# Optimization experiments

Hardware: AMD Instinct MI355X
Metric: run time of the kernel (lower is better)

The kernel has to match this reference:

```python
import jax, jax.numpy as jnp
import numpy as np

K = 32  # k-th nearest neighbor (excluding self), matches KDistanceDetector(k=32)


def setup_inputs() -> dict:
    key = jax.random.key(0)
    B, D = 16384, 128
    images = jax.random.normal(key, (B, D), dtype=jnp.float32)
    return {"images": images}


def reference(images):
    # model is identity: vision_features = images, shape [B, D]
    x = images
    # torch.cdist p=2 with mm path: sq dists via gram matrix
    sq_norms = jnp.sum(x * x, axis=1)                      # [B]
    sq = sq_norms[:, None] + sq_norms[None, :] - 2.0 * (x @ x.T)  # [B, B]
    sq = jnp.maximum(sq, 0.0)
    B = x.shape[0]
    # Mask out the diagonal (self-distance). Original removes it and views
    # [B, B-1]; setting it to +inf before sorting yields the identical k-th
    # smallest value (inf sorts last), and keeps sqrt grads clean.
    diag = jnp.eye(B, dtype=bool)
    sq = jnp.where(diag, jnp.inf, sq)
    d = jnp.sqrt(sq)                                       # [B, B]
    a = jnp.sort(d, axis=1)                                # full per-row sort, as in original
    return a[:, K]                                         # [B]
```

## Files before the change

### kernel.cpp

```cpp
#include <hip/hip_runtime.h>


typedef unsigned short u16;
typedef unsigned int   u32;
typedef __attribute__((ext_vector_type(8))) u16    ushort8;
typedef __attribute__((ext_vector_type(8))) __bf16 bf16x8;
typedef __attribute__((ext_vector_type(4))) float  f32x4;
typedef __attribute__((ext_vector_type(4))) u32    u32x4;

#define NB   16384
#define ND   128
#define NSEG 32
#define SCAP 12
#define NTH  33
#define ZWH  (-2.62f)
#define NEGF (-3.0e38f)
#define POSF ( 3.0e38f)
#define NPB  64
#define NPBL 256

#define OFF_X    ((size_t)0)
#define OFF_NORM (OFF_X    + (size_t)NB * ND * 2)
#define OFF_TACC (OFF_NORM + (size_t)NB * 4)
#define OFF_PART (OFF_TACC + (size_t)NB * 4)
#define OFF_CNTS (OFF_PART + (size_t)NPBL * 130 * 4)
#define OFF_CAND (OFF_CNTS + (size_t)NB * NSEG * 4)

static __device__ __forceinline__ u16 f2bf(float f) {
  u32 u = __float_as_uint(f);
  u32 r = u + 0x7FFFu + ((u >> 16) & 1u);
  return (u16)(r >> 16);
}
static __device__ __forceinline__ float bf2f(u16 h) {
  return __uint_as_float(((u32)h) << 16);
}

#if defined(__has_builtin)
#if __has_builtin(__builtin_amdgcn_global_load_lds)
#define HAVE_GLDS 1
#endif
#endif

static __device__ __forceinline__ void stage16(const u16* gsrc_lane,
                                               u16* lds_base, int l) {
#ifdef HAVE_GLDS
  __builtin_amdgcn_global_load_lds(
      (const __attribute__((address_space(1))) void*)gsrc_lane,
      (__attribute__((address_space(3))) void*)lds_base, 16, 0, 0);
#else
  *(ushort8*)(lds_base + l * 8) = *(const ushort8*)gsrc_lane;
#endif
}
static __device__ __forceinline__ void stage4(const float* gsrc_lane,
                                              float* lds_base, int l) {
#ifdef HAVE_GLDS
  __builtin_amdgcn_global_load_lds(
      (const __attribute__((address_space(1))) void*)gsrc_lane,
      (__attribute__((address_space(3))) void*)lds_base, 4, 0, 0);
#else
  lds_base[l] = *gsrc_lane;
#endif
}

__global__ void k_prepstats(const float* __restrict__ x, u16* __restrict__ X,
                            float* __restrict__ norms, float* __restrict__ partial) {
  __shared__ float xs[16][128];
  __shared__ float red1[256], red2[256];
  int t = threadIdx.x;
  int cg = t & 15;
  int rs = t >> 4;
  int rbase = blockIdx.x * NPB;
  float cs[8] = {0.f, 0.f, 0.f, 0.f, 0.f, 0.f, 0.f, 0.f};
  float s1 = 0.f, s2 = 0.f;
#pragma unroll
  for (int rr = 0; rr < NPB / 16; ++rr) {
    int row = rbase + rs + rr * 16;
    const float* src = x + (size_t)row * ND + cg * 8;
    float4 a0 = *(const float4*)(src);
    float4 a1 = *(const float4*)(src + 4);
    float v[8] = {a0.x, a0.y, a0.z, a0.w, a1.x, a1.y, a1.z, a1.w};
    ushort8 pack;
    float ns = 0.f;
#pragma unroll
    for (int u = 0; u < 8; ++u) {
      u16 h = f2bf(v[u]);
      float b = bf2f(h);
      pack[u] = h;
      ns += b * b;
      cs[u] += b;
    }
    *(ushort8*)(X + (size_t)row * ND + cg * 8) = pack;
#pragma unroll
    for (int off = 1; off < 16; off <<= 1) ns += __shfl_xor(ns, off, 64);
    if (cg == 0) { norms[row] = ns; s1 += ns; s2 += ns * ns; }
  }
#pragma unroll
  for (int u = 0; u < 8; ++u) xs[rs][cg * 8 + u] = cs[u];
  red1[t] = s1; red2[t] = s2;
  __syncthreads();
  if (t < 128) {
    float a = 0.f;
    for (int r2 = 0; r2 < 16; ++r2) a += xs[r2][t];
    partial[(size_t)blockIdx.x * 130 + t] = a;
  }
  for (int st = 128; st > 0; st >>= 1) {
    if (t < st) { red1[t] += red1[t + st]; red2[t] += red2[t + st]; }
    __syncthreads();
  }
  if (t == 0) {
    partial[(size_t)blockIdx.x * 130 + 128] = red1[0];
    partial[(size_t)blockIdx.x * 130 + 129] = red2[0];
  }
}

__global__ void k_thresh(const u16* __restrict__ X, const float* __restrict__ norms,
                         const float* __restrict__ partial, float* __restrict__ tacc) {
  __shared__ float xb[128];
  __shared__ float ssum[2];
  int t = threadIdx.x;
  if (t < 128) {
    float a = 0.f;
    for (int b = 0; b < NPBL; ++b) a += partial[(size_t)b * 130 + t];
    xb[t] = a * (1.0f / NB);
  } else if (t == 128 || t == 129) {
    float a = 0.f;
    for (int b = 0; b < NPBL; ++b) a += partial[(size_t)b * 130 + t];
    ssum[t - 128] = a;
  }
  __syncthreads();
  int r = blockIdx.x * 256 + t;
  float n = norms[r];
  const u16* xr = X + (size_t)r * ND;
  float dot = 0.f;
#pragma unroll
  for (int c8 = 0; c8 < 16; ++c8) {
    ushort8 v = *(const ushort8*)(xr + c8 * 8);
#pragma unroll
    for (int j = 0; j < 8; ++j) dot += bf2f(v[j]) * xb[c8 * 8 + j];
  }
  float nbar = ssum[0] * (1.0f / NB);
  float Vn = fmaxf(ssum[1] * (1.0f / NB) - nbar * nbar, 0.f);
  float m = n + nbar - 2.f * dot;
  float v = Vn + 4.f * n * (nbar / ND);
  float nu = 2.f * m * m / v;
  float cc = v / (2.f * m);
  float a1 = 2.f / (9.f * nu);
  float inner = 1.f - a1 + ZWH * sqrtf(a1);
  float tsq = cc * nu * inner * inner * inner;
  tacc[r] = 0.5f * (n - tsq);
}

__global__ __launch_bounds__(512, 4) void k_gram(
    const u16* __restrict__ X, const float* __restrict__ norms,
    const float* __restrict__ tacc, u32* __restrict__ counts,
    float* __restrict__ cands) {
  __shared__ u16 ldsA[2][32 * 512];
  __shared__ __align__(16) float nchs[2][128];
  const int bid = blockIdx.x;
  const int logical = (bid & 7) * 64 + (bid >> 3);
  const int q = logical >> 7, strip = logical & 127;
  const int r0 = strip * 128;
  const int t = threadIdx.x, w = t >> 6, l = t & 63;
  const int wr = w >> 1, wc = w & 1;
  const int lm = l & 15, lq = l >> 4;
  const int koff = lq * 8;

  bf16x8 bfrag[4][2];
#pragma unroll
  for (int k = 0; k < 4; ++k)
#pragma unroll
    for (int j = 0; j < 2; ++j)
      bfrag[k][j] = __builtin_bit_cast(bf16x8, *(const ushort8*)(
          X + (size_t)(r0 + wr * 32 + j * 16 + lm) * ND + k * 32 + koff));

  int rj[2]; float tj[2]; u32 cnt2[2]; u32 segb[2];
#pragma unroll
  for (int j = 0; j < 2; ++j) {
    rj[j] = r0 + wr * 32 + j * 16 + lm;
    tj[j] = tacc[rj[j]];
    cnt2[j] = 0;
    segb[j] = (u32)(rj[j] * NSEG + q * 8 + wc * 4 + lq) * SCAP;
  }

  {
    const int c0 = q * 4096;
#pragma unroll
    for (int s = 0; s < 4; ++s) {
      int g = w * 4 + s;
      stage16(X + (size_t)(c0 + (g & 7) * 16 + lm) * ND + (g >> 3) * 32 + koff,
              &ldsA[0][g * 512], l);
    }
    if (w < 2) stage4(norms + c0 + w * 64 + l, &nchs[0][w * 64], l);
  }
  __syncthreads();

  for (int it = 0; it < 32; ++it) {
    const int cur = it & 1;
    const int c0 = q * 4096 + it * 128;
    if (it + 1 < 32) {
      const int c1 = c0 + 128;
      u16* dstA = ldsA[cur ^ 1];
#pragma unroll
      for (int s = 0; s < 4; ++s) {
        int g = w * 4 + s;
        stage16(X + (size_t)(c1 + (g & 7) * 16 + lm) * ND + (g >> 3) * 32 + koff,
                &dstA[g * 512], l);
      }
      if (w < 2) stage4(norms + c1 + w * 64 + l, &nchs[cur ^ 1][w * 64], l);
    }
    __builtin_amdgcn_sched_barrier(0);

    f32x4 acc[4][2];
#pragma unroll
    for (int i = 0; i < 4; ++i)
#pragma unroll
      for (int j = 0; j < 2; ++j) acc[i][j] = (f32x4){0.f, 0.f, 0.f, 0.f};

    const u16* srcA = ldsA[cur];
#pragma unroll
    for (int k = 0; k < 4; ++k) {
      bf16x8 af[4];
#pragma unroll
      for (int i = 0; i < 4; ++i)
        af[i] = __builtin_bit_cast(bf16x8,
                 *(const ushort8*)(&srcA[(k * 8 + wc * 4 + i) * 512 + l * 8]));
#pragma unroll
      for (int i = 0; i < 4; ++i)
#pragma unroll
        for (int j = 0; j < 2; ++j)
          acc[i][j] = __builtin_amdgcn_mfma_f32_16x16x32_bf16(af[i], bfrag[k][j], acc[i][j], 0, 0, 0);
    }

    f32x4 nch4[4];
#pragma unroll
    for (int i = 0; i < 4; ++i) {
      nch4[i] = *(const f32x4*)(&nchs[cur][wc * 64 + i * 16 + lq * 4]);
      nch4[i] = nch4[i] * 0.5f;
    }

    const bool dg = (c0 == r0);
#pragma unroll
    for (int i = 0; i < 4; ++i) {
#pragma unroll
      for (int j = 0; j < 2; ++j) {
#pragma unroll
        for (int v = 0; v < 4; ++v) {
          float val = acc[i][j][v] - nch4[i][v];
          bool p = (val >= tj[j]);
          if (dg) p = p && ((c0 + wc * 64 + i * 16 + lq * 4 + v) != rj[j]);
          if (p) {
            u32 c = cnt2[j];
            if (c < SCAP) cands[segb[j] + c] = val;
            cnt2[j] = c + 1;
          }
        }
      }
    }

    __syncthreads();
  }
#pragma unroll
  for (int j = 0; j < 2; ++j)
    counts[rj[j] * NSEG + q * 8 + wc * 4 + lq] = cnt2[j];
}

__global__ void k_select(const u32* __restrict__ counts, const float* __restrict__ cands,
                         const float* __restrict__ norms, float* __restrict__ out) {
  int w = threadIdx.x >> 6, l = threadIdx.x & 63;
  int r = blockIdx.x * 4 + w;
  u32 myc = (l < NSEG) ? counts[r * NSEG + l] : 0u;
  u32 tot = myc, mx = myc;
#pragma unroll
  for (int off = 1; off < 64; off <<= 1) {
    tot += __shfl_xor(tot, off, 64);
    u32 o = (u32)__shfl_xor((int)mx, off, 64);
    mx = mx > o ? mx : o;
  }
  if (tot < NTH || mx > SCAP) return;

  const float* base = cands + (size_t)r * (NSEG * SCAP);
  float v0, v1, v2, v3, v4, v5;
#define LOADV(e, dst)                                        \
  {                                                          \
    int f = l + 64 * e;                                      \
    int sg = f / SCAP, sl = f - sg * SCAP;                   \
    u32 c = (u32)__shfl((int)myc, sg, 64);                   \
    float x = base[f];                                       \
    dst = (sl < (int)c) ? x : NEGF;                          \
  }
  LOADV(0, v0) LOADV(1, v1) LOADV(2, v2) LOADV(3, v3) LOADV(4, v4) LOADV(5, v5)
#undef LOADV

  float last = NEGF;
  for (int e = 0; e < NTH; ++e) {
    float m = fmaxf(fmaxf(fmaxf(v0, v1), fmaxf(v2, v3)), fmaxf(v4, v5));
#pragma unroll
    for (int off = 1; off < 64; off <<= 1) m = fmaxf(m, __shfl_xor(m, off, 64));
    bool mine = (v0 == m) || (v1 == m) || (v2 == m) || (v3 == m) || (v4 == m) || (v5 == m);
    unsigned long long bal = __ballot(mine);
    int owner = __ffsll(bal) - 1;
    if (l == owner) {
      if      (v0 == m) v0 = NEGF;
      else if (v1 == m) v1 = NEGF;
      else if (v2 == m) v2 = NEGF;
      else if (v3 == m) v3 = NEGF;
      else if (v4 == m) v4 = NEGF;
      else              v5 = NEGF;
    }
    last = m;
  }
  out[r] = sqrtf(fmaxf(norms[r] - 2.f * last, 0.f));
}

__global__ void k_fallback(const u32* __restrict__ counts, const u16* __restrict__ X,
                           const float* __restrict__ norms, float* __restrict__ out) {
  __shared__ float sq[NB];
  __shared__ float xr[ND];
  __shared__ float rmin[256];
  __shared__ int   ridx[256];
  __shared__ float tmin[256];
  __shared__ int   tidx[256];
  __shared__ int   nbad;
  __shared__ int   badlist[256];
  int t = threadIdx.x;
  if (t == 0) nbad = 0;
  __syncthreads();
  int r = blockIdx.x * 256 + t;
  u32 tot = 0, mx = 0;
#pragma unroll
  for (int s4 = 0; s4 < 8; ++s4) {
    u32x4 c = *(const u32x4*)(counts + (size_t)r * NSEG + s4 * 4);
#pragma unroll
    for (int u = 0; u < 4; ++u) { tot += c[u]; mx = c[u] > mx ? c[u] : mx; }
  }
  if (tot < NTH || mx > SCAP) { int p = atomicAdd(&nbad, 1); badlist[p] = r; }
  __syncthreads();
  int nb = nbad;
  for (int ii = 0; ii < nb; ++ii) {
    int rr = badlist[ii];
    if (t < 128) xr[t] = bf2f(X[(size_t)rr * ND + t]);
    __syncthreads();
    float n_r = norms[rr];
    for (int jj = 0; jj < 64; ++jj) {
      int j = t + 256 * jj;
      const u16* xj = X + (size_t)j * ND;
      float dot = 0.f;
#pragma unroll
      for (int c8 = 0; c8 < 16; ++c8) {
        ushort8 vv = *(const ushort8*)(xj + c8 * 8);
#pragma unroll
        for (int u = 0; u < 8; ++u) dot += bf2f(vv[u]) * xr[c8 * 8 + u];
      }
      sq[j] = (j == rr) ? POSF : fmaxf(n_r + norms[j] - 2.f * dot, 0.f);
    }
    __syncthreads();
    {
      float lmv = POSF; int lix = -1;
      for (int jj = 0; jj < 64; ++jj) {
        int j = t + 256 * jj;
        float s = sq[j];
        if (s < lmv) { lmv = s; lix = j; }
      }
      rmin[t] = lmv; ridx[t] = lix;
    }
    __syncthreads();
    float last = 0.f;
    for (int e = 0; e < NTH; ++e) {
      tmin[t] = rmin[t]; tidx[t] = ridx[t];
      __syncthreads();
      for (int s = 128; s > 0; s >>= 1) {
        if (t < s && tmin[t + s] < tmin[t]) { tmin[t] = tmin[t + s]; tidx[t] = tidx[t + s]; }
        __syncthreads();
      }
      float gm = tmin[0]; int gi = tidx[0];
      last = gm;
      __syncthreads();
      if (t == (gi & 255)) {
        sq[gi] = POSF;
        float lmv = POSF; int lix = -1;
        for (int jj = 0; jj < 64; ++jj) {
          int j = t + 256 * jj;
          float s = sq[j];
          if (s < lmv) { lmv = s; lix = j; }
        }
        rmin[t] = lmv; ridx[t] = lix;
      }
      __syncthreads();
    }
    if (t == 0) out[rr] = sqrtf(fmaxf(last, 0.f));
    __syncthreads();
  }
}

extern "C" void kernel_launch(void* const* d_in, const int* in_sizes, int n_in,
                              void* d_out, int out_size, void* d_ws, size_t ws_size,
                              hipStream_t stream) {
  const float* x = (const float*)d_in[0];
  float* out = (float*)d_out;
  char* ws = (char*)d_ws;
  u16*   X     = (u16*)  (ws + OFF_X);
  float* norms = (float*)(ws + OFF_NORM);
  float* tacc  = (float*)(ws + OFF_TACC);
  float* part  = (float*)(ws + OFF_PART);
  u32*   cnts  = (u32*)  (ws + OFF_CNTS);
  float* cands = (float*)(ws + OFF_CAND);

  k_prepstats<<<NPBL, 256, 0, stream>>>(x, X, norms, part);
  k_thresh   <<<64,   256, 0, stream>>>(X, norms, part, tacc);
  k_gram     <<<512,  512, 0, stream>>>(X, norms, tacc, cnts, cands);
  k_select   <<<4096, 256, 0, stream>>>(cnts, cands, norms, out);
  k_fallback <<<64,   256, 0, stream>>>(cnts, X, norms, out);
}
```

Measured before the change: 181.5 us.

## Software-pipeline candidate filtering one tile behind MFMA computation in gram kernel

Each iteration now issues the MFMAs for the current column tile, then runs the threshold filter and candidate stores on the previous tile's accumulators, so the filter ALU work can overlap with MFMA latency. The norm staging buffer grows to four slots so the previous tile's norms stay valid, and a final epilogue filters the last tile. This costs 32 extra accumulator registers per thread, which may raise register pressure and hurt occupancy at the 512x4 launch bounds.

```diff
diff --git a/kernel.cpp b/kernel.cpp
--- a/kernel.cpp
+++ b/kernel.cpp
@@ -150,12 +150,31 @@
   tacc[r] = 0.5f * (n - tsq);
 }
 
+#define FILTER_PREV(ACC, NCH, C0P)                                            \
+  {                                                                           \
+    const bool dgp = ((C0P) == r0);                                           \
+    _Pragma("unroll") for (int i = 0; i < 4; ++i) {                           \
+      _Pragma("unroll") for (int j = 0; j < 2; ++j) {                         \
+        _Pragma("unroll") for (int v = 0; v < 4; ++v) {                       \
+          float val = (ACC)[i][j][v] - (NCH)[i][v];                           \
+          bool p = (val >= tj[j]);                                            \
+          if (dgp) p = p && (((C0P) + wc * 64 + i * 16 + lq * 4 + v) != rj[j]); \
+          if (p) {                                                            \
+            u32 c = cnt2[j];                                                  \
+            if (c < SCAP) cands[segb[j] + c] = val;                           \
+            cnt2[j] = c + 1;                                                  \
+          }                                                                   \
+        }                                                                     \
+      }                                                                       \
+    }                                                                         \
+  }
+
 __global__ __launch_bounds__(512, 4) void k_gram(
     const u16* __restrict__ X, const float* __restrict__ norms,
     const float* __restrict__ tacc, u32* __restrict__ counts,
     float* __restrict__ cands) {
   __shared__ u16 ldsA[2][32 * 512];
-  __shared__ __align__(16) float nchs[2][128];
+  __shared__ __align__(16) float nchs[4][128];
   const int bid = blockIdx.x;
   const int logical = (bid & 7) * 64 + (bid >> 3);
   const int q = logical >> 7, strip = logical & 127;
@@ -194,6 +213,9 @@
   }
   __syncthreads();
 
+  f32x4 accP[4][2];
+  int c0p = 0;
+
   for (int it = 0; it < 32; ++it) {
     const int cur = it & 1;
     const int c0 = q * 4096 + it * 128;
@@ -206,15 +228,15 @@
         stage16(X + (size_t)(c1 + (g & 7) * 16 + lm) * ND + (g >> 3) * 32 + koff,
                 &dstA[g * 512], l);
       }
-      if (w < 2) stage4(norms + c1 + w * 64 + l, &nchs[cur ^ 1][w * 64], l);
+      if (w < 2) stage4(norms + c1 + w * 64 + l, &nchs[(it + 1) & 3][w * 64], l);
     }
     __builtin_amdgcn_sched_barrier(0);
 
-    f32x4 acc[4][2];
+    f32x4 accC[4][2];
 #pragma unroll
     for (int i = 0; i < 4; ++i)
 #pragma unroll
-      for (int j = 0; j < 2; ++j) acc[i][j] = (f32x4){0.f, 0.f, 0.f, 0.f};
+      for (int j = 0; j < 2; ++j) accC[i][j] = (f32x4){0.f, 0.f, 0.f, 0.f};
 
     const u16* srcA = ldsA[cur];
 #pragma unroll
@@ -228,37 +250,40 @@
       for (int i = 0; i < 4; ++i)
 #pragma unroll
         for (int j = 0; j < 2; ++j)
-          acc[i][j] = __builtin_amdgcn_mfma_f32_16x16x32_bf16(af[i], bfrag[k][j], acc[i][j], 0, 0, 0);
-    }
-
+          accC[i][j] = __builtin_amdgcn_mfma_f32_16x16x32_bf16(af[i], bfrag[k][j], accC[i][j], 0, 0, 0);
+    }
+
+    if (it > 0) {
+      const int pb = (it - 1) & 3;
+      f32x4 nch4[4];
+#pragma unroll
+      for (int i = 0; i < 4; ++i) {
+        nch4[i] = *(const f32x4*)(&nchs[pb][wc * 64 + i * 16 + lq * 4]);
+        nch4[i] = nch4[i] * 0.5f;
+      }
+      FILTER_PREV(accP, nch4, c0p)
+    }
+
+#pragma unroll
+    for (int i = 0; i < 4; ++i)
+#pragma unroll
+      for (int j = 0; j < 2; ++j) accP[i][j] = accC[i][j];
+    c0p = c0;
+
+    __syncthreads();
+  }
+
+  {
+    const int pb = 31 & 3;
     f32x4 nch4[4];
 #pragma unroll
     for (int i = 0; i < 4; ++i) {
-      nch4[i] = *(const f32x4*)(&nchs[cur][wc * 64 + i * 16 + lq * 4]);
+      nch4[i] = *(const f32x4*)(&nchs[pb][wc * 64 + i * 16 + lq * 4]);
       nch4[i] = nch4[i] * 0.5f;
     }
-
-    const bool dg = (c0 == r0);
-#pragma unroll
-    for (int i = 0; i < 4; ++i) {
-#pragma unroll
-      for (int j = 0; j < 2; ++j) {
-#pragma unroll
-        for (int v = 0; v < 4; ++v) {
-          float val = acc[i][j][v] - nch4[i][v];
-          bool p = (val >= tj[j]);
-          if (dg) p = p && ((c0 + wc * 64 + i * 16 + lq * 4 + v) != rj[j]);
-          if (p) {
-            u32 c = cnt2[j];
-            if (c < SCAP) cands[segb[j] + c] = val;
-            cnt2[j] = c + 1;
-          }
-        }
-      }
-    }
-
-    __syncthreads();
-  }
+    FILTER_PREV(accP, nch4, c0p)
+  }
+
 #pragma unroll
   for (int j = 0; j < 2; ++j)
     counts[rj[j] * NSEG + q * 8 + wc * 4 + lq] = cnt2[j];
```

Result: slower. 210.1 us (+15.7%).

## Restructure gram loop per row-tile and read norms directly from global

Applied to the files above, without the earlier changes.

The inner loop now handles one 16-column tile at a time: it loads its A fragments, runs the four k-step MFMAs into a small two-element accumulator, and filters candidates right away, instead of holding a 4x2 accumulator array across all k-steps. The column norms are read straight from global memory per tile rather than staged into a double-buffered LDS array. This lowers accumulator register pressure and removes the LDS staging, which could help occupancy. In exchange there are shorter MFMA dependency chains per tile, less overlap between MFMA and the filter code, and global norm loads that sit on the critical path.

```diff
diff --git a/kernel.cpp b/kernel.cpp
--- a/kernel.cpp
+++ b/kernel.cpp
@@ -49,16 +49,6 @@
       (__attribute__((address_space(3))) void*)lds_base, 16, 0, 0);
 #else
   *(ushort8*)(lds_base + l * 8) = *(const ushort8*)gsrc_lane;
-#endif
-}
-static __device__ __forceinline__ void stage4(const float* gsrc_lane,
-                                              float* lds_base, int l) {
-#ifdef HAVE_GLDS
-  __builtin_amdgcn_global_load_lds(
-      (const __attribute__((address_space(1))) void*)gsrc_lane,
-      (__attribute__((address_space(3))) void*)lds_base, 4, 0, 0);
-#else
-  lds_base[l] = *gsrc_lane;
 #endif
 }
 
@@ -155,7 +145,6 @@
     const float* __restrict__ tacc, u32* __restrict__ counts,
     float* __restrict__ cands) {
   __shared__ u16 ldsA[2][32 * 512];
-  __shared__ __align__(16) float nchs[2][128];
   const int bid = blockIdx.x;
   const int logical = (bid & 7) * 64 + (bid >> 3);
   const int q = logical >> 7, strip = logical & 127;
@@ -190,7 +179,6 @@
       stage16(X + (size_t)(c0 + (g & 7) * 16 + lm) * ND + (g >> 3) * 32 + koff,
               &ldsA[0][g * 512], l);
     }
-    if (w < 2) stage4(norms + c0 + w * 64 + l, &nchs[0][w * 64], l);
   }
   __syncthreads();
 
@@ -206,46 +194,34 @@
         stage16(X + (size_t)(c1 + (g & 7) * 16 + lm) * ND + (g >> 3) * 32 + koff,
                 &dstA[g * 512], l);
       }
-      if (w < 2) stage4(norms + c1 + w * 64 + l, &nchs[cur ^ 1][w * 64], l);
     }
     __builtin_amdgcn_sched_barrier(0);
 
-    f32x4 acc[4][2];
-#pragma unroll
-    for (int i = 0; i < 4; ++i)
-#pragma unroll
-      for (int j = 0; j < 2; ++j) acc[i][j] = (f32x4){0.f, 0.f, 0.f, 0.f};
-
     const u16* srcA = ldsA[cur];
-#pragma unroll
-    for (int k = 0; k < 4; ++k) {
+    const bool dg = (c0 == r0);
+
+#pragma unroll
+    for (int i = 0; i < 4; ++i) {
+      f32x4 nch = *(const f32x4*)(norms + c0 + wc * 64 + i * 16 + lq * 4);
       bf16x8 af[4];
 #pragma unroll
-      for (int i = 0; i < 4; ++i)
-        af[i] = __builtin_bit_cast(bf16x8,
+      for (int k = 0; k < 4; ++k)
+        af[k] = __builtin_bit_cast(bf16x8,
                  *(const ushort8*)(&srcA[(k * 8 + wc * 4 + i) * 512 + l * 8]));
-#pragma unroll
-      for (int i = 0; i < 4; ++i)
+      f32x4 acc[2];
+#pragma unroll
+      for (int j = 0; j < 2; ++j) acc[j] = (f32x4){0.f, 0.f, 0.f, 0.f};
+#pragma unroll
+      for (int k = 0; k < 4; ++k)
 #pragma unroll
         for (int j = 0; j < 2; ++j)
-          acc[i][j] = __builtin_amdgcn_mfma_f32_16x16x32_bf16(af[i], bfrag[k][j], acc[i][j], 0, 0, 0);
-    }
-
-    f32x4 nch4[4];
-#pragma unroll
-    for (int i = 0; i < 4; ++i) {
-      nch4[i] = *(const f32x4*)(&nchs[cur][wc * 64 + i * 16 + lq * 4]);
-      nch4[i] = nch4[i] * 0.5f;
-    }
-
-    const bool dg = (c0 == r0);
-#pragma unroll
-    for (int i = 0; i < 4; ++i) {
+          acc[j] = __builtin_amdgcn_mfma_f32_16x16x32_bf16(af[k], bfrag[k][j], acc[j], 0, 0, 0);
+      nch = nch * 0.5f;
 #pragma unroll
       for (int j = 0; j < 2; ++j) {
 #pragma unroll
         for (int v = 0; v < 4; ++v) {
-          float val = acc[i][j][v] - nch4[i][v];
+          float val = acc[j][v] - nch[v];
           bool p = (val >= tj[j]);
           if (dg) p = p && ((c0 + wc * 64 + i * 16 + lq * 4 + v) != rj[j]);
           if (p) {
```

After: 204.0 us. 12.4% more time.
